# Optimization experiments

Hardware: AMD Instinct MI355X
Metric: run time of the kernel (lower is better)

## Reference

```python
import jax, jax.numpy as jnp
import numpy as np

TEMPERATURE = 0.07


def setup_inputs() -> dict:
    key = jax.random.key(0)
    embeddings = jax.random.normal(key, (16384, 256), dtype=jnp.float32)
    return {"embeddings": embeddings}


def reference(embeddings) -> jnp.ndarray:
    # L2 normalize rows (torch F.normalize uses eps clamp 1e-12)
    norm = jnp.maximum(jnp.linalg.norm(embeddings, axis=1, keepdims=True), 1e-12)
    emb = embeddings / norm
    # [N, N] similarity, temperature-scaled logits
    logits = jnp.matmul(emb, emb.T) / TEMPERATURE
    # cross entropy against diagonal labels (labels[i] = i)
    logp = jax.nn.log_softmax(logits, axis=1)
    loss = -jnp.mean(jnp.diagonal(logp))
    return loss
```

## Files before the change

kernel.cpp:

```cpp
#include <hip/hip_runtime.h>
#include <hip/hip_bf16.h>

typedef __bf16 bf16;
typedef __attribute__((ext_vector_type(8))) __bf16 bf16x8;
typedef __attribute__((ext_vector_type(4))) __bf16 bf16x4;
typedef __attribute__((ext_vector_type(16))) float f32x16;

#define N_ROWS 16384
#define DIM 256
#define NT 128
#define NJC 256
#define LSTRIP 8
#define NSTRIPS 2112
#define SQK1 4.53981608f
#define LN2F 0.69314718056f

#define WS_T_OFF (N_ROWS * DIM * 2)
#define WS_D_OFF (WS_T_OFF + N_ROWS * 4)

#define GLOAD_LDS(g, l)                                        \
    __builtin_amdgcn_global_load_lds(                          \
        (const __attribute__((address_space(1))) void*)(g),    \
        (__attribute__((address_space(3))) void*)(l), 16, 0, 0)

__global__ void __launch_bounds__(256) normalize_kernel(const float* __restrict__ in,
                                                        bf16* __restrict__ out,
                                                        float* __restrict__ Tg,
                                                        float* __restrict__ Dg,
                                                        float* __restrict__ loss_out) {
    if (blockIdx.x == 0 && threadIdx.x == 0) loss_out[0] = 0.0f;
    if (blockIdx.x < 64) Tg[blockIdx.x * 256 + threadIdx.x] = 0.0f;

    const int row  = blockIdx.x * 4 + (threadIdx.x >> 6);
    const int lane = threadIdx.x & 63;
    const float4* rp = (const float4*)(in + (size_t)row * DIM);
    float4 v = rp[lane];
    float ss = v.x * v.x + v.y * v.y + v.z * v.z + v.w * v.w;
#pragma unroll
    for (int m = 1; m < 64; m <<= 1) ss += __shfl_xor(ss, m, 64);
    float inv = SQK1 / fmaxf(sqrtf(ss), 1e-12f);
    bf16x4 o;
    o[0] = (bf16)(v.x * inv);
    o[1] = (bf16)(v.y * inv);
    o[2] = (bf16)(v.z * inv);
    o[3] = (bf16)(v.w * inv);
    *(bf16x4*)(out + (size_t)row * DIM + lane * 4) = o;

    float f0 = (float)o[0], f1 = (float)o[1], f2 = (float)o[2], f3 = (float)o[3];
    float s2 = f0 * f0 + f1 * f1 + f2 * f2 + f3 * f3;
#pragma unroll
    for (int m = 1; m < 64; m <<= 1) s2 += __shfl_xor(s2, m, 64);
    if (lane == 0) Dg[row] = s2;
}

#define TREE16(R, out)                                                     \
    do {                                                                   \
        float w8[8], w4[4], w2[2], w1, g_;                                 \
        _Pragma("unroll") for (int i_ = 0; i_ < 8; ++i_) {                 \
            g_ = (lo & 16) ? R[i_] : R[i_ + 8];                            \
            w8[i_] = ((lo & 16) ? R[i_ + 8] : R[i_]) + __shfl_xor(g_, 16); \
        }                                                                  \
        _Pragma("unroll") for (int i_ = 0; i_ < 4; ++i_) {                 \
            g_ = (lo & 8) ? w8[i_] : w8[i_ + 4];                           \
            w4[i_] = ((lo & 8) ? w8[i_ + 4] : w8[i_]) + __shfl_xor(g_, 8); \
        }                                                                  \
        _Pragma("unroll") for (int i_ = 0; i_ < 2; ++i_) {                 \
            g_ = (lo & 4) ? w4[i_] : w4[i_ + 2];                           \
            w2[i_] = ((lo & 4) ? w4[i_ + 2] : w4[i_]) + __shfl_xor(g_, 4); \
        }                                                                  \
        g_ = (lo & 2) ? w2[0] : w2[1];                                     \
        w1 = ((lo & 2) ? w2[1] : w2[0]) + __shfl_xor(g_, 2);               \
        out = w1 + __shfl_xor(w1, 1);                                      \
    } while (0)

__global__ void __launch_bounds__(512, 4)
loss_kernel(const bf16* __restrict__ A, float* __restrict__ Tg) {
    __shared__ bf16 Bs0[64 * DIM];
    __shared__ bf16 Bs1[64 * DIM];
    __shared__ float CsAcc[4][LSTRIP][64];

    const int tid = threadIdx.x;
    const int w  = tid >> 6;
    const int l  = tid & 63;
    const int lo = l & 31, hi = l >> 5;
    const int rg = w >> 1;
    const int cg = w & 1;

    int it = 0, rem = blockIdx.x;
    for (;;) {
        int nch = (NJC - 2 * it + LSTRIP - 1) >> 3;
        if (rem < nch) break;
        rem -= nch;
        ++it;
    }
    const int jc0 = 2 * it + rem * LSTRIP;
    const int jc1 = (jc0 + LSTRIP < NJC) ? (jc0 + LSTRIP) : NJC;

    bf16x8 af[16];
    {
        const bf16* ap = A + (size_t)(it * 128 + rg * 32 + lo) * DIM + hi * 8;
#pragma unroll
        for (int k = 0; k < 16; ++k)
            af[k] = *(const volatile bf16x8*)(ap + k * 16);
    }

    float s0[16];
#pragma unroll
    for (int r = 0; r < 16; ++r) s0[r] = 0.f;

    const int s_dma = l & 31;
    const int rl    = l >> 5;
    int vo[4];
#pragma unroll
    for (int q = 0; q < 4; ++q) {
        const int c = (s_dma & 24) | ((s_dma & 7) ^ ((q * 2 + rl) & 7));
        vo[q] = rl * DIM + c * 8;
    }

    const int rbase = (cg * 32 + lo) * DIM;
    const int mx7 = lo & 7;

#define ISSUE(jcn, BUF)                                                      \
    do {                                                                     \
        const bf16* tb_ = A + (size_t)((jcn) * 64 + w * 8) * DIM;            \
        bf16* lb_ = &BUF[(w * 8) * DIM];                                     \
        _Pragma("unroll") for (int q_ = 0; q_ < 4; ++q_) {                   \
            GLOAD_LDS(tb_ + (q_ * 2) * DIM + vo[q_],                         \
                      lb_ + (q_ * 2) * DIM);                                 \
        }                                                                    \
    } while (0)

#define TILE_BODY(BR, BW, jc, t)                                             \
    do {                                                                     \
        asm volatile("s_barrier" ::: "memory");                              \
        if ((jc) + 1 < jc1) {                                                \
            ISSUE((jc) + 1, BW);                                             \
            asm volatile("s_waitcnt vmcnt(4)" ::: "memory");                 \
        } else {                                                             \
            asm volatile("s_waitcnt vmcnt(0)" ::: "memory");                 \
        }                                                                    \
        asm volatile("s_barrier" ::: "memory");                              \
        f32x16 c0;                                                           \
        _Pragma("unroll") for (int r_ = 0; r_ < 16; ++r_) c0[r_] = 0.f;      \
        _Pragma("unroll") for (int k_ = 0; k_ < 16; ++k_) {                  \
            const int cc_ = k_ * 2 + hi;                                     \
            const int slot_ = (cc_ & 24) | ((cc_ & 7) ^ mx7);                \
            bf16x8 b_ = *(const bf16x8*)&BR[rbase + slot_ * 8];              \
            c0 = __builtin_amdgcn_mfma_f32_32x32x16_bf16(af[k_], b_, c0, 0, 0, 0); \
        }                                                                    \
        float cs_ = 0.f;                                                     \
        _Pragma("unroll") for (int r_ = 0; r_ < 16; ++r_) {                  \
            float e_ = __builtin_amdgcn_exp2f(c0[r_]);                       \
            s0[r_] += e_;                                                    \
            cs_ += e_;                                                       \
        }                                                                    \
        cs_ += __shfl_xor(cs_, 32);                                          \
        if (hi == 0) CsAcc[rg][t][cg * 32 + lo] = cs_;                       \
    } while (0)

    ISSUE(jc0, Bs0);
    int jc = jc0;
    while (jc < jc1) {
        TILE_BODY(Bs0, Bs1, jc, jc - jc0);
        ++jc;
        if (jc >= jc1) break;
        TILE_BODY(Bs1, Bs0, jc, jc - jc0);
        ++jc;
    }

    float t0;
    TREE16(s0, t0);
    const int r = (lo >> 1) & 15;
    const int rowoff = (r & 3) + 8 * (r >> 2) + 4 * hi;
    if ((l & 1) == 0)
        atomicAdd(&Tg[it * 128 + rg * 32 + rowoff], t0);

    __syncthreads();
    const int nt_strip = jc1 - jc0;
    for (int i = tid; i < nt_strip * 64; i += 512) {
        const int t = i >> 6, col = i & 63;
        if (((jc0 + t) >> 1) != it) {
            atomicAdd(&Tg[(jc0 + t) * 64 + col],
                      CsAcc[0][t][col] + CsAcc[1][t][col] +
                      CsAcc[2][t][col] + CsAcc[3][t][col]);
        }
    }
#undef ISSUE
#undef TILE_BODY
}

__global__ void __launch_bounds__(256) final_kernel(const float* __restrict__ Tg,
                                                    const float* __restrict__ Dg,
                                                    float* __restrict__ out) {
    __shared__ float red[4];
    const int i = blockIdx.x * 256 + threadIdx.x;
    float c = LN2F * (__log2f(Tg[i]) - Dg[i]) * (1.0f / (float)N_ROWS);
#pragma unroll
    for (int m = 1; m < 64; m <<= 1) c += __shfl_xor(c, m, 64);
    if ((threadIdx.x & 63) == 0) red[threadIdx.x >> 6] = c;
    __syncthreads();
    if (threadIdx.x == 0)
        atomicAdd(out, red[0] + red[1] + red[2] + red[3]);
}

extern "C" void kernel_launch(void* const* d_in, const int* in_sizes, int n_in,
                              void* d_out, int out_size, void* d_ws, size_t ws_size,
                              hipStream_t stream) {
    const float* emb = (const float*)d_in[0];
    float* out = (float*)d_out;
    bf16* Abf = (bf16*)d_ws;
    float* Tg = (float*)((char*)d_ws + WS_T_OFF);
    float* Dg = (float*)((char*)d_ws + WS_D_OFF);

    hipLaunchKernelGGL(normalize_kernel, dim3(N_ROWS / 4), dim3(256), 0, stream,
                       emb, Abf, Tg, Dg, out);
    hipLaunchKernelGGL(loss_kernel, dim3(NSTRIPS), dim3(512), 0, stream,
                       Abf, Tg);
    hipLaunchKernelGGL(final_kernel, dim3(N_ROWS / 256), dim3(256), 0, stream,
                       Tg, Dg, out);
}
```

Before: 167.7 us.

## Fuse final reduction into loss kernel via last-block counter and widen strips

Drops the separate final kernel launch. The last loss block, found through an atomic done counter, now computes the log-sum and writes the loss. Strip length doubles from 8 to 16 tiles, which halves the number of blocks and amortizes the A-fragment load and the atomics across more tiles. Column sums are now accumulated with LDS atomics into one shared array instead of four per-group slots. The trade-off is a serial tail: one block reads all 16K rows at the end, and fewer blocks may balance less evenly across CUs.

```diff
diff --git a/kernel.cpp b/kernel.cpp
--- a/kernel.cpp
+++ b/kernel.cpp
@@ -10,13 +10,14 @@
 #define DIM 256
 #define NT 128
 #define NJC 256
-#define LSTRIP 8
-#define NSTRIPS 2112
+#define LSTRIP 16
+#define NSTRIPS 1088
 #define SQK1 4.53981608f
 #define LN2F 0.69314718056f
 
 #define WS_T_OFF (N_ROWS * DIM * 2)
 #define WS_D_OFF (WS_T_OFF + N_ROWS * 4)
+#define WS_DONE_OFF (WS_D_OFF + N_ROWS * 4)
 
 #define GLOAD_LDS(g, l)                                        \
     __builtin_amdgcn_global_load_lds(                          \
@@ -27,8 +28,9 @@
                                                         bf16* __restrict__ out,
                                                         float* __restrict__ Tg,
                                                         float* __restrict__ Dg,
+                                                        int* __restrict__ done,
                                                         float* __restrict__ loss_out) {
-    if (blockIdx.x == 0 && threadIdx.x == 0) loss_out[0] = 0.0f;
+    if (blockIdx.x == 0 && threadIdx.x == 0) { loss_out[0] = 0.0f; done[0] = 0; }
     if (blockIdx.x < 64) Tg[blockIdx.x * 256 + threadIdx.x] = 0.0f;
 
     const int row  = blockIdx.x * 4 + (threadIdx.x >> 6);
@@ -74,10 +76,14 @@
     } while (0)
 
 __global__ void __launch_bounds__(512, 4)
-loss_kernel(const bf16* __restrict__ A, float* __restrict__ Tg) {
+loss_kernel(const bf16* __restrict__ A, float* __restrict__ Tg,
+            const float* __restrict__ Dg, int* __restrict__ done,
+            float* __restrict__ loss_out) {
     __shared__ bf16 Bs0[64 * DIM];
     __shared__ bf16 Bs1[64 * DIM];
-    __shared__ float CsAcc[4][LSTRIP][64];
+    __shared__ float CsAcc[LSTRIP][64];
+    __shared__ float red2[8];
+    __shared__ int lastflag;
 
     const int tid = threadIdx.x;
     const int w  = tid >> 6;
@@ -88,7 +94,7 @@
 
     int it = 0, rem = blockIdx.x;
     for (;;) {
-        int nch = (NJC - 2 * it + LSTRIP - 1) >> 3;
+        int nch = (NJC - 2 * it + LSTRIP - 1) >> 4;
         if (rem < nch) break;
         rem -= nch;
         ++it;
@@ -101,12 +107,15 @@
         const bf16* ap = A + (size_t)(it * 128 + rg * 32 + lo) * DIM + hi * 8;
 #pragma unroll
         for (int k = 0; k < 16; ++k)
-            af[k] = *(const volatile bf16x8*)(ap + k * 16);
+            af[k] = *(const bf16x8*)(ap + k * 16);
     }
 
     float s0[16];
 #pragma unroll
     for (int r = 0; r < 16; ++r) s0[r] = 0.f;
+
+    for (int i = tid; i < LSTRIP * 64; i += 512) ((float*)CsAcc)[i] = 0.f;
+    __syncthreads();
 
     const int s_dma = l & 31;
     const int rl    = l >> 5;
@@ -155,7 +164,7 @@
             cs_ += e_;                                                       \
         }                                                                    \
         cs_ += __shfl_xor(cs_, 32);                                          \
-        if (hi == 0) CsAcc[rg][t][cg * 32 + lo] = cs_;                       \
+        if (hi == 0) atomicAdd(&CsAcc[t][cg * 32 + lo], cs_);                \
     } while (0)
 
     ISSUE(jc0, Bs0);
@@ -179,28 +188,36 @@
     const int nt_strip = jc1 - jc0;
     for (int i = tid; i < nt_strip * 64; i += 512) {
         const int t = i >> 6, col = i & 63;
-        if (((jc0 + t) >> 1) != it) {
-            atomicAdd(&Tg[(jc0 + t) * 64 + col],
-                      CsAcc[0][t][col] + CsAcc[1][t][col] +
-                      CsAcc[2][t][col] + CsAcc[3][t][col]);
+        if (((jc0 + t) >> 1) != it)
+            atomicAdd(&Tg[(jc0 + t) * 64 + col], CsAcc[t][col]);
+    }
+
+    __syncthreads();
+    if (tid == 0) {
+        int old = __hip_atomic_fetch_add(done, 1, __ATOMIC_ACQ_REL,
+                                         __HIP_MEMORY_SCOPE_AGENT);
+        lastflag = (old == NSTRIPS - 1);
+    }
+    __syncthreads();
+    if (lastflag) {
+        float acc = 0.f;
+        for (int i = tid; i < N_ROWS; i += 512) {
+            float t = __hip_atomic_load(&Tg[i], __ATOMIC_RELAXED,
+                                        __HIP_MEMORY_SCOPE_AGENT);
+            acc += __log2f(t) - Dg[i];
+        }
+#pragma unroll
+        for (int m = 1; m < 64; m <<= 1) acc += __shfl_xor(acc, m, 64);
+        if (l == 0) red2[w] = acc;
+        __syncthreads();
+        if (tid == 0) {
+            float s = red2[0] + red2[1] + red2[2] + red2[3] +
+                      red2[4] + red2[5] + red2[6] + red2[7];
+            loss_out[0] = LN2F * s * (1.0f / (float)N_ROWS);
         }
     }
 #undef ISSUE
 #undef TILE_BODY
-}
-
-__global__ void __launch_bounds__(256) final_kernel(const float* __restrict__ Tg,
-                                                    const float* __restrict__ Dg,
-                                                    float* __restrict__ out) {
-    __shared__ float red[4];
-    const int i = blockIdx.x * 256 + threadIdx.x;
-    float c = LN2F * (__log2f(Tg[i]) - Dg[i]) * (1.0f / (float)N_ROWS);
-#pragma unroll
-    for (int m = 1; m < 64; m <<= 1) c += __shfl_xor(c, m, 64);
-    if ((threadIdx.x & 63) == 0) red[threadIdx.x >> 6] = c;
-    __syncthreads();
-    if (threadIdx.x == 0)
-        atomicAdd(out, red[0] + red[1] + red[2] + red[3]);
 }
 
 extern "C" void kernel_launch(void* const* d_in, const int* in_sizes, int n_in,
@@ -211,11 +228,10 @@
     bf16* Abf = (bf16*)d_ws;
     float* Tg = (float*)((char*)d_ws + WS_T_OFF);
     float* Dg = (float*)((char*)d_ws + WS_D_OFF);
+    int* done = (int*)((char*)d_ws + WS_DONE_OFF);
 
     hipLaunchKernelGGL(normalize_kernel, dim3(N_ROWS / 4), dim3(256), 0, stream,
-                       emb, Abf, Tg, Dg, out);
+                       emb, Abf, Tg, Dg, done, out);
     hipLaunchKernelGGL(loss_kernel, dim3(NSTRIPS), dim3(512), 0, stream,
-                       Abf, Tg);
-    hipLaunchKernelGGL(final_kernel, dim3(N_ROWS / 256), dim3(256), 0, stream,
-                       Tg, Dg, out);
+                       Abf, Tg, Dg, done, out);
 }
```

Measured after the change: 189.5 us. 13.0% more time.
